# Optimization experiments

Hardware: AMD Instinct MI355X
Metric: run time of the kernel (lower is better)

The kernel has to match this reference:

```python
import jax, jax.numpy as jnp
import numpy as np
import math

D = 1024      # hidden_size
H = 16        # num_heads
HD = D // H   # head_dim = 64
ROPE = 64     # rope_dim == head_dim (full-head rotation, empty pass-through)
E = 8         # num_experts
F = 2560
BASE = 10000.0
EPS = 1e-5
SPECIALS = jnp.arange(2, 8)  # special_tokens indices {2..7} used as global tokens


def _ln(x, w, b):
    m = x.mean(-1, keepdims=True)
    v = x.var(-1, keepdims=True)  # biased var, matches torch LayerNorm
    return (x - m) / jnp.sqrt(v + EPS) * w + b


def _rope(x, cos, sin):
    # x: [B,H,T,HD]; rotate first ROPE dims via half-split (NOT rotate-half interleave)
    x1, x2 = x[..., : ROPE // 2], x[..., ROPE // 2 : ROPE]
    rot = jnp.concatenate([x1 * cos - x2 * sin, x1 * sin + x2 * cos], axis=-1)
    return jnp.concatenate([rot, x[..., ROPE:]], axis=-1)


def setup_inputs() -> dict:
    key = jax.random.key(0)
    ks = jax.random.split(key, 8)
    B, T = 1, 1024
    g = lambda k, shape, s: (jax.random.normal(k, shape, jnp.float32) * s)
    return {
        "x": g(ks[0], (B, T, D), 1.0),
        "input_ids": jax.random.randint(ks[1], (B, T), 0, 32000),
        "ln1_w": jnp.ones((D,), jnp.float32), "ln1_b": jnp.zeros((D,), jnp.float32),
        "qkv_w": g(ks[2], (D, 3 * D), 0.02), "qkv_b": jnp.zeros((3 * D,), jnp.float32),
        "attn_out_w": g(ks[3], (D, D), 0.02), "attn_out_b": jnp.zeros((D,), jnp.float32),
        "ln2_w": jnp.ones((D,), jnp.float32), "ln2_b": jnp.zeros((D,), jnp.float32),
        "gate_w": g(ks[4], (D, E), 0.02), "gate_b": jnp.zeros((E,), jnp.float32),
        "fc_w": g(ks[5], (E, D, 2 * F), 0.02), "fc_b": jnp.zeros((E, 2 * F), jnp.float32),
        "eout_w": g(ks[6], (E, F, D), 0.02), "eout_b": jnp.zeros((E, D), jnp.float32),
    }


def _block(x, input_ids, ln1_w, ln1_b, qkv_w, qkv_b, attn_out_w, attn_out_b,
           ln2_w, ln2_b, gate_w, gate_b, fc_w, fc_b, eout_w, eout_b):
    B, T, _ = x.shape
    # --- self-attention (pre-norm) ---
    h = _ln(x, ln1_w, ln1_b)
    qkv = h @ qkv_w + qkv_b
    q, k, v = jnp.split(qkv, 3, axis=-1)
    resh = lambda t: t.reshape(B, T, H, HD).transpose(0, 2, 1, 3)  # [B,H,T,HD]
    q, k, v = resh(q), resh(k), resh(v)
    pos = jnp.arange(T, dtype=jnp.float32)
    inv = 1.0 / (BASE ** (jnp.arange(0, ROPE, 2, dtype=jnp.float32) / ROPE))
    fr = pos[:, None] * inv[None, :]            # [T, ROPE/2]
    cos, sin = jnp.cos(fr), jnp.sin(fr)
    q = _rope(q, cos, sin)
    k = _rope(k, cos, sin)
    causal = jnp.tril(jnp.ones((T, T), bool))
    glob = (input_ids[..., None] == SPECIALS).any(-1)            # [B,T]
    allowed = causal[None, None] | glob[:, None, :, None]        # [B,1,T,T]
    logits = jnp.einsum('bhqd,bhkd->bhqk', q, k) / math.sqrt(HD)
    neg = -jnp.finfo(logits.dtype).max
    logits = jnp.where(allowed, logits, neg)
    aw = jax.nn.softmax(logits, axis=-1)
    attn = jnp.einsum('bhqk,bhkd->bhqd', aw, v).transpose(0, 2, 1, 3).reshape(B, T, H * HD)
    x = x + (attn @ attn_out_w + attn_out_b)
    # --- MoE GEGLU FFN (hard top-1 routing) ---
    h2 = _ln(x, ln2_w, ln2_b)
    gp = jax.nn.softmax(h2 @ gate_w + gate_b, axis=-1)           # [B,T,E]
    gw = gp.max(-1)
    gi = gp.argmax(-1)
    xf = h2.reshape(-1, D)
    gif = gi.reshape(-1)
    gwf = gw.reshape(-1)
    N = xf.shape[0]
    outf = jnp.zeros((N, D), x.dtype)
    for e in range(E):  # fixed small expert loop; select by routing mask
        h12 = xf @ fc_w[e] + fc_b[e]
        x1, x2 = h12[:, :F], h12[:, F:]
        y = (x1 * jax.nn.gelu(x2, approximate=False)) @ eout_w[e] + eout_b[e]
        outf = outf + jnp.where((gif == e)[:, None], y, 0.0)
    outf = outf * gwf[:, None]
    sums = jax.ops.segment_sum(gwf, gif, num_segments=E)
    counts = jax.ops.segment_sum(jnp.ones_like(gwf), gif, num_segments=E)
    usage = sums / (counts + 1e-8)
    moe_loss = jnp.sum((usage - 1.0 / E) ** 2)
    return x + outf.reshape(B, T, D), moe_loss


def reference(x, input_ids, ln1_w, ln1_b, qkv_w, qkv_b, attn_out_w, attn_out_b,
              ln2_w, ln2_b, gate_w, gate_b, fc_w, fc_b, eout_w, eout_b):
    return _block(x, input_ids, ln1_w, ln1_b, qkv_w, qkv_b, attn_out_w, attn_out_b,
                  ln2_w, ln2_b, gate_w, gate_b, fc_w, fc_b, eout_w, eout_b)
```

## Files before the change

### kernel.cpp

```cpp
#include <hip/hip_runtime.h>
#include <float.h>
#include <math.h>
#include <stdint.h>

#define T_ 1024
#define D_ 1024
#define H_ 16
#define HD_ 64
#define E_ 8
#define F_ 2560
#define D3_ 3072
#define F2_ 5120

#define WS_H    0u
#define WS_QKV  1048576u
#define WS_ATTN 4194304u
#define WS_X2   5242880u
#define WS_H2   6291456u
#define WS_A    7340032u
#define WS_GW   9961472u
#define WS_GI   9962496u
#define WS_OFFS 9963520u
#define WS_PERM 9963536u

typedef short short8 __attribute__((ext_vector_type(8)));
typedef short short4v __attribute__((ext_vector_type(4)));
typedef __bf16 bf16x8 __attribute__((ext_vector_type(8)));
typedef float floatx4 __attribute__((ext_vector_type(4)));

union FragU { short8 s; bf16x8 b; };

__device__ __forceinline__ short f2bf(float f) {
    union { float f; uint32_t u; } a; a.f = f;
    uint32_t r = a.u + 0x7fffu + ((a.u >> 16) & 1u);
    return (short)(r >> 16);
}

__device__ __forceinline__ void cvt16(const float4& a0, const float4& a1,
                                      const float4& a2, const float4& a3,
                                      short8& c0, short8& c1) {
    c0[0]=f2bf(a0.x); c0[1]=f2bf(a0.y); c0[2]=f2bf(a0.z); c0[3]=f2bf(a0.w);
    c0[4]=f2bf(a1.x); c0[5]=f2bf(a1.y); c0[6]=f2bf(a1.z); c0[7]=f2bf(a1.w);
    c1[0]=f2bf(a2.x); c1[1]=f2bf(a2.y); c1[2]=f2bf(a2.z); c1[3]=f2bf(a2.w);
    c1[4]=f2bf(a3.x); c1[5]=f2bf(a3.y); c1[6]=f2bf(a3.z); c1[7]=f2bf(a3.w);
}

#define GEMM_IDS \
    const int tid  = threadIdx.x;                 \
    const int a_m  = tid >> 1;                    \
    const int a_kh = (tid & 1) * 16;              \
    const int lane = tid & 63, wave = tid >> 6;   \
    const int wm = wave & 1,  wn = wave >> 1;     \
    const int quad = lane >> 4, lm = lane & 15;

__global__ __launch_bounds__(256) void gemm_mfma_full(
    const float* __restrict__ A, int lda,
    const float* __restrict__ B, int ldb,
    const float* __restrict__ bias,
    float* __restrict__ C, int ldc, int K)
{
    __shared__ __align__(16) short As[4*128*8];
    __shared__ __align__(16) short Bs[64*40];
    const int row0 = blockIdx.y * 128, col0 = blockIdx.x * 64;
    GEMM_IDS
    const int b_n = tid >> 2, b_kc = tid & 3;
    floatx4 acc[4][2];
    #pragma unroll
    for (int i=0;i<4;i++)
        #pragma unroll
        for (int j=0;j<2;j++) acc[i][j] = (floatx4){0.f,0.f,0.f,0.f};

    const float* apx = A + (size_t)(row0 + a_m) * lda + a_kh;
    const float* bpx = B + (size_t)(b_kc*8) * ldb + col0 + b_n;
    const int kcA = (tid & 1) * 2;

    float4 a0, a1, a2, a3; float bvv[8];
    a0 = *(const float4*)(apx);     a1 = *(const float4*)(apx + 4);
    a2 = *(const float4*)(apx + 8); a3 = *(const float4*)(apx + 12);
    #pragma unroll
    for (int j=0;j<8;j++) bvv[j] = bpx[(size_t)j*ldb];

    for (int k0 = 0; k0 < K; k0 += 32) {
        __syncthreads();
        short8 c0, c1, cb;
        cvt16(a0,a1,a2,a3,c0,c1);
        #pragma unroll
        for (int j=0;j<8;j++) cb[j] = f2bf(bvv[j]);
        *(short8*)&As[((kcA  )*128 + a_m)*8] = c0;
        *(short8*)&As[((kcA+1)*128 + a_m)*8] = c1;
        *(short8*)&Bs[b_n*40 + b_kc*8] = cb;
        __syncthreads();
        if (k0 + 32 < K) {
            const float* ap2 = apx + k0 + 32;
            a0 = *(const float4*)(ap2);     a1 = *(const float4*)(ap2 + 4);
            a2 = *(const float4*)(ap2 + 8); a3 = *(const float4*)(ap2 + 12);
            const float* bp2 = bpx + (size_t)(k0+32) * ldb;
            #pragma unroll
            for (int j=0;j<8;j++) bvv[j] = bp2[(size_t)j*ldb];
        }
        FragU fa[4], fb[2];
        #pragma unroll
        for (int i=0;i<4;i++) fa[i].s = *(short8*)&As[(quad*128 + wm*64 + i*16 + lm)*8];
        #pragma unroll
        for (int j=0;j<2;j++) fb[j].s = *(short8*)&Bs[(wn*32 + j*16 + lm)*40 + quad*8];
        #pragma unroll
        for (int i=0;i<4;i++)
            #pragma unroll
            for (int j=0;j<2;j++)
                acc[i][j] = __builtin_amdgcn_mfma_f32_16x16x32_bf16(fa[i].b, fb[j].b, acc[i][j], 0,0,0);
    }
    #pragma unroll
    for (int i=0;i<4;i++)
        #pragma unroll
        for (int j=0;j<2;j++) {
            int col = col0 + wn*32 + j*16 + lm;
            float bb = bias ? bias[col] : 0.f;
            #pragma unroll
            for (int r=0;r<4;r++) {
                int row = row0 + wm*64 + i*16 + quad*4 + r;
                C[(size_t)row*ldc + col] = acc[i][j][r] + bb;
            }
        }
}

__global__ __launch_bounds__(256) void gemm_mfma_acc(
    const float* __restrict__ A, int lda,
    const float* __restrict__ B, int ldb, long sB,
    const int* __restrict__ offs, const int* __restrict__ perm,
    float* __restrict__ Cacc, int ldc, int K, int nsk)
{
    const int sk = blockIdx.z % nsk;
    const int e  = blockIdx.z / nsk;
    int off = 0, Ne = T_;
    if (offs) { off = offs[e]; Ne = offs[e+1] - off; }
    const int row0 = blockIdx.y * 128;
    if (row0 >= Ne) return;
    const int col0 = blockIdx.x * 64;
    B += (long)e * sB;

    __shared__ __align__(16) short As[4*128*8];
    __shared__ __align__(16) short Bs[64*40];
    __shared__ int toks[128];
    GEMM_IDS
    const int b_n = tid >> 2, b_kc = tid & 3;
    if (tid < 128) {
        int r = row0 + tid;
        toks[tid] = offs ? ((r < Ne) ? perm[off + r] : -1) : r;
    }
    __syncthreads();

    floatx4 acc[4][2];
    #pragma unroll
    for (int i=0;i<4;i++)
        #pragma unroll
        for (int j=0;j<2;j++) acc[i][j] = (floatx4){0.f,0.f,0.f,0.f};

    const int tokA = toks[a_m];
    const float* apx = (tokA >= 0) ? (A + (size_t)tokA * lda + a_kh) : nullptr;
    const float* bpx = B + (size_t)(b_kc*8) * ldb + col0 + b_n;
    const int kcA = (tid & 1) * 2;
    const int Kp = K / nsk;
    const int koff = sk * Kp, kend = koff + Kp;

    float4 a0, a1, a2, a3; float bvv[8];
    a0 = make_float4(0,0,0,0); a1 = a0; a2 = a0; a3 = a0;
    if (apx) {
        a0 = *(const float4*)(apx + koff);     a1 = *(const float4*)(apx + koff + 4);
        a2 = *(const float4*)(apx + koff + 8); a3 = *(const float4*)(apx + koff + 12);
    }
    {
        const float* bp2 = bpx + (size_t)koff * ldb;
        #pragma unroll
        for (int j=0;j<8;j++) bvv[j] = bp2[(size_t)j*ldb];
    }

    for (int k0 = koff; k0 < kend; k0 += 32) {
        __syncthreads();
        short8 c0, c1, cb;
        cvt16(a0,a1,a2,a3,c0,c1);
        #pragma unroll
        for (int j=0;j<8;j++) cb[j] = f2bf(bvv[j]);
        *(short8*)&As[((kcA  )*128 + a_m)*8] = c0;
        *(short8*)&As[((kcA+1)*128 + a_m)*8] = c1;
        *(short8*)&Bs[b_n*40 + b_kc*8] = cb;
        __syncthreads();
        if (k0 + 32 < kend) {
            if (apx) {
                const float* ap2 = apx + k0 + 32;
                a0 = *(const float4*)(ap2);     a1 = *(const float4*)(ap2 + 4);
                a2 = *(const float4*)(ap2 + 8); a3 = *(const float4*)(ap2 + 12);
            }
            const float* bp2 = bpx + (size_t)(k0+32) * ldb;
            #pragma unroll
            for (int j=0;j<8;j++) bvv[j] = bp2[(size_t)j*ldb];
        }
        FragU fa[4], fb[2];
        #pragma unroll
        for (int i=0;i<4;i++) fa[i].s = *(short8*)&As[(quad*128 + wm*64 + i*16 + lm)*8];
        #pragma unroll
        for (int j=0;j<2;j++) fb[j].s = *(short8*)&Bs[(wn*32 + j*16 + lm)*40 + quad*8];
        #pragma unroll
        for (int i=0;i<4;i++)
            #pragma unroll
            for (int j=0;j<2;j++)
                acc[i][j] = __builtin_amdgcn_mfma_f32_16x16x32_bf16(fa[i].b, fb[j].b, acc[i][j], 0,0,0);
    }
    #pragma unroll
    for (int i=0;i<4;i++)
        #pragma unroll
        for (int j=0;j<2;j++) {
            int col = col0 + wn*32 + j*16 + lm;
            #pragma unroll
            for (int r=0;r<4;r++) {
                int tk = toks[wm*64 + i*16 + quad*4 + r];
                if (tk >= 0) atomicAdd(&Cacc[(size_t)tk*ldc + col], acc[i][j][r]);
            }
        }
}

__global__ __launch_bounds__(256) void moe_fc_mfma(
    const float* __restrict__ h2, const float* __restrict__ fcw,
    const float* __restrict__ fcb, const int* __restrict__ offs,
    const int* __restrict__ perm, float* __restrict__ aout)
{
    const int e = blockIdx.z;
    const int off = offs[e];
    const int Ne = offs[e+1] - off;
    const int row0 = blockIdx.y * 128;
    if (row0 >= Ne) return;
    const int col0 = blockIdx.x * 32;

    __shared__ __align__(16) short As[4*128*8];
    __shared__ __align__(16) short B1s[32*40];
    __shared__ __align__(16) short B2s[32*40];
    __shared__ int toks[128];
    GEMM_IDS
    const int n_l = tid & 31, kg = tid >> 5;
    if (tid < 128) {
        int r = row0 + tid;
        toks[tid] = (r < Ne) ? perm[off + r] : -1;
    }
    __syncthreads();

    floatx4 acc1[4], acc2[4];
    #pragma unroll
    for (int i=0;i<4;i++) {
        acc1[i] = (floatx4){0.f,0.f,0.f,0.f};
        acc2[i] = (floatx4){0.f,0.f,0.f,0.f};
    }

    const float* W = fcw + (size_t)e * D_ * F2_;
    const int tokA = toks[a_m];
    const float* apx = (tokA >= 0) ? (h2 + (size_t)tokA * D_ + a_kh) : nullptr;
    const float* bpx = W + (size_t)(kg*4) * F2_ + col0 + n_l;
    const int kcA = (tid & 1) * 2;

    float4 a0, a1, a2, a3; float b1v[4], b2v[4];
    a0 = make_float4(0,0,0,0); a1 = a0; a2 = a0; a3 = a0;
    if (apx) {
        a0 = *(const float4*)(apx);     a1 = *(const float4*)(apx + 4);
        a2 = *(const float4*)(apx + 8); a3 = *(const float4*)(apx + 12);
    }
    #pragma unroll
    for (int j=0;j<4;j++) { b1v[j] = bpx[(size_t)j*F2_]; b2v[j] = bpx[(size_t)j*F2_ + F_]; }

    for (int k0 = 0; k0 < D_; k0 += 32) {
        __syncthreads();
        short8 c0, c1;
        short4v cb1, cb2;
        cvt16(a0,a1,a2,a3,c0,c1);
        #pragma unroll
        for (int j=0;j<4;j++) { cb1[j] = f2bf(b1v[j]); cb2[j] = f2bf(b2v[j]); }
        *(short8*)&As[((kcA  )*128 + a_m)*8] = c0;
        *(short8*)&As[((kcA+1)*128 + a_m)*8] = c1;
        *(short4v*)&B1s[n_l*40 + kg*4] = cb1;
        *(short4v*)&B2s[n_l*40 + kg*4] = cb2;
        __syncthreads();
        if (k0 + 32 < D_) {
            if (apx) {
                const float* ap2 = apx + k0 + 32;
                a0 = *(const float4*)(ap2);     a1 = *(const float4*)(ap2 + 4);
                a2 = *(const float4*)(ap2 + 8); a3 = *(const float4*)(ap2 + 12);
            }
            const float* bp2 = bpx + (size_t)(k0+32) * F2_;
            #pragma unroll
            for (int j=0;j<4;j++) { b1v[j] = bp2[(size_t)j*F2_]; b2v[j] = bp2[(size_t)j*F2_ + F_]; }
        }
        FragU fa[4], fb1, fb2;
        #pragma unroll
        for (int i=0;i<4;i++) fa[i].s = *(short8*)&As[(quad*128 + wm*64 + i*16 + lm)*8];
        fb1.s = *(short8*)&B1s[(wn*16 + lm)*40 + quad*8];
        fb2.s = *(short8*)&B2s[(wn*16 + lm)*40 + quad*8];
        #pragma unroll
        for (int i=0;i<4;i++) {
            acc1[i] = __builtin_amdgcn_mfma_f32_16x16x32_bf16(fa[i].b, fb1.b, acc1[i], 0,0,0);
            acc2[i] = __builtin_amdgcn_mfma_f32_16x16x32_bf16(fa[i].b, fb2.b, acc2[i], 0,0,0);
        }
    }
    {
        int col = col0 + wn*16 + lm;
        float b1 = fcb[(size_t)e*F2_ + col];
        float b2 = fcb[(size_t)e*F2_ + F_ + col];
        #pragma unroll
        for (int i=0;i<4;i++)
            #pragma unroll
            for (int r=0;r<4;r++) {
                int tk = toks[wm*64 + i*16 + quad*4 + r];
                if (tk < 0) continue;
                float v1 = acc1[i][r] + b1;
                float v2 = acc2[i][r] + b2;
                float g = v2 * 0.5f * (1.0f + erff(v2 * 0.70710678118654752f));
                aout[(size_t)tk*F_ + col] = v1 * g;
            }
    }
}

__global__ __launch_bounds__(128) void flash_attn(
    const float* __restrict__ qkv, const int* __restrict__ ids,
    float* __restrict__ attnout)
{
    const int h  = blockIdx.y;
    const int q0 = blockIdx.x * 32;
    const int tid = threadIdx.x;
    const int lane = tid & 63, w = tid >> 6;
    const int quad = lane >> 4, lm = lane & 15;

    __shared__ __align__(16) short Qs[32*72];
    __shared__ __align__(16) short Ks[64*72];
    __shared__ __align__(16) short Vt[64*72];
    __shared__ __align__(16) short Ps[2][16*72];
    __shared__ int globf[32];

    {
        int row = tid >> 2, c = (tid & 3) * 16;
        const float* qp = qkv + (size_t)(q0 + row) * D3_ + h * HD_ + c;
        float4 f0 = *(const float4*)(qp);
        float4 f1 = *(const float4*)(qp + 4);
        float4 f2 = *(const float4*)(qp + 8);
        float4 f3 = *(const float4*)(qp + 12);
        short8 s0, s1;
        cvt16(f0, f1, f2, f3, s0, s1);
        *(short8*)&Qs[row*72 + c]     = s0;
        *(short8*)&Qs[row*72 + c + 8] = s1;
    }
    if (tid < 32) {
        int id = ids[q0 + tid];
        globf[tid] = (id >= 2 && id <= 7) ? 1 : 0;
    }
    __syncthreads();

    FragU QA[2];
    #pragma unroll
    for (int s = 0; s < 2; s++)
        QA[s].s = *(short8*)&Qs[(w*16 + lm)*72 + s*32 + quad*8];

    int any = 0;
    #pragma unroll
    for (int i = 0; i < 32; i++) any |= globf[i];
    const int nt = any ? (T_/64) : ((q0 + 31) >> 6) + 1;

    int gq[4]; int qidx[4];
    #pragma unroll
    for (int r = 0; r < 4; r++) {
        int ql = w*16 + quad*4 + r;
        qidx[r] = q0 + ql;
        gq[r] = globf[ql];
    }

    float mrow[4] = {-1e30f, -1e30f, -1e30f, -1e30f};
    float lrow[4] = {0.f, 0.f, 0.f, 0.f};
    floatx4 Oacc[4];
    #pragma unroll
    for (int n = 0; n < 4; n++) Oacc[n] = (floatx4){0.f, 0.f, 0.f, 0.f};

    for (int kt = 0; kt < nt; kt++) {
        __syncthreads();
        #pragma unroll
        for (int rep = 0; rep < 2; rep++) {
            int key = (tid >> 2) + rep*32;
            int c = (tid & 3) * 16;
            const float* kp = qkv + (size_t)(kt*64 + key) * D3_ + D_ + h*HD_ + c;
            float4 f0 = *(const float4*)(kp);
            float4 f1 = *(const float4*)(kp + 4);
            float4 f2 = *(const float4*)(kp + 8);
            float4 f3 = *(const float4*)(kp + 12);
            short8 s0, s1;
            cvt16(f0, f1, f2, f3, s0, s1);
            *(short8*)&Ks[key*72 + c]     = s0;
            *(short8*)&Ks[key*72 + c + 8] = s1;
        }
        #pragma unroll
        for (int rep = 0; rep < 8; rep++) {
            int lin = tid + rep*128;
            int key = lin >> 4;
            int c = (lin & 15) * 4;
            const float* vp = qkv + (size_t)(kt*64 + key) * D3_ + 2*D_ + h*HD_ + c;
            float4 f = *(const float4*)vp;
            Vt[(c+0)*72 + key] = f2bf(f.x);
            Vt[(c+1)*72 + key] = f2bf(f.y);
            Vt[(c+2)*72 + key] = f2bf(f.z);
            Vt[(c+3)*72 + key] = f2bf(f.w);
        }
        __syncthreads();

        floatx4 Sv[4];
        #pragma unroll
        for (int n = 0; n < 4; n++) {
            Sv[n] = (floatx4){0.f, 0.f, 0.f, 0.f};
            #pragma unroll
            for (int s = 0; s < 2; s++) {
                FragU KB;
                KB.s = *(short8*)&Ks[(n*16 + lm)*72 + s*32 + quad*8];
                Sv[n] = __builtin_amdgcn_mfma_f32_16x16x32_bf16(QA[s].b, KB.b, Sv[n], 0, 0, 0);
            }
        }
        #pragma unroll
        for (int n = 0; n < 4; n++) {
            int key = kt*64 + n*16 + lm;
            #pragma unroll
            for (int r = 0; r < 4; r++) {
                float v = Sv[n][r] * 0.125f;
                if (!gq[r] && key > qidx[r]) v = -1e30f;
                Sv[n][r] = v;
            }
        }
        float mnew[4], alpha[4], tsum[4];
        #pragma unroll
        for (int r = 0; r < 4; r++) {
            float tm = fmaxf(fmaxf(Sv[0][r], Sv[1][r]), fmaxf(Sv[2][r], Sv[3][r]));
            #pragma unroll
            for (int x = 1; x < 16; x <<= 1) tm = fmaxf(tm, __shfl_xor(tm, x));
            mnew[r] = fmaxf(mrow[r], tm);
            alpha[r] = __expf(mrow[r] - mnew[r]);
            mrow[r] = mnew[r];
            tsum[r] = 0.f;
        }
        #pragma unroll
        for (int n = 0; n < 4; n++) {
            #pragma unroll
            for (int r = 0; r < 4; r++) {
                float p = __expf(Sv[n][r] - mnew[r]);
                tsum[r] += p;
                Ps[w][(quad*4 + r)*72 + n*16 + lm] = f2bf(p);
            }
        }
        #pragma unroll
        for (int r = 0; r < 4; r++) {
            #pragma unroll
            for (int x = 1; x < 16; x <<= 1) tsum[r] += __shfl_xor(tsum[r], x);
            lrow[r] = lrow[r] * alpha[r] + tsum[r];
        }
        #pragma unroll
        for (int n = 0; n < 4; n++)
            #pragma unroll
            for (int r = 0; r < 4; r++) Oacc[n][r] *= alpha[r];

        #pragma unroll
        for (int s = 0; s < 2; s++) {
            FragU PA;
            PA.s = *(short8*)&Ps[w][lm*72 + s*32 + quad*8];
            #pragma unroll
            for (int n = 0; n < 4; n++) {
                FragU VB;
                VB.s = *(short8*)&Vt[(n*16 + lm)*72 + s*32 + quad*8];
                Oacc[n] = __builtin_amdgcn_mfma_f32_16x16x32_bf16(PA.b, VB.b, Oacc[n], 0, 0, 0);
            }
        }
    }

    #pragma unroll
    for (int n = 0; n < 4; n++)
        #pragma unroll
        for (int r = 0; r < 4; r++) {
            float o = Oacc[n][r] / lrow[r];
            attnout[(size_t)qidx[r]*D_ + h*HD_ + n*16 + lm] = o;
        }
}

__global__ __launch_bounds__(256) void ep_attn(
    const float* __restrict__ x, const float* __restrict__ sacc,
    const float* __restrict__ aob, float* __restrict__ x2)
{
    int row = blockIdx.x, tid = threadIdx.x;
    float4 xv = ((const float4*)(x + (size_t)row*D_))[tid];
    float4 sv = ((const float4*)(sacc + (size_t)row*D_))[tid];
    float4 bv = ((const float4*)aob)[tid];
    float4 o;
    o.x = xv.x + sv.x + bv.x; o.y = xv.y + sv.y + bv.y;
    o.z = xv.z + sv.z + bv.z; o.w = xv.w + sv.w + bv.w;
    ((float4*)(x2 + (size_t)row*D_))[tid] = o;
}

__global__ __launch_bounds__(256) void ep_moe(
    const float* __restrict__ x2, const float* __restrict__ sacc,
    const float* __restrict__ eob, const float* __restrict__ gw,
    const int* __restrict__ gi, float* __restrict__ out)
{
    int row = blockIdx.x, tid = threadIdx.x;
    float g = gw[row];
    int e = gi[row];
    float4 xv = ((const float4*)(x2 + (size_t)row*D_))[tid];
    float4 sv = ((const float4*)(sacc + (size_t)row*D_))[tid];
    float4 bv = ((const float4*)(eob + (size_t)e*D_))[tid];
    float4 o;
    o.x = xv.x + g*(sv.x + bv.x); o.y = xv.y + g*(sv.y + bv.y);
    o.z = xv.z + g*(sv.z + bv.z); o.w = xv.w + g*(sv.w + bv.w);
    ((float4*)(out + (size_t)row*D_))[tid] = o;
}

__global__ __launch_bounds__(256) void ln_kernel(
    const float* __restrict__ x, const float* __restrict__ w,
    const float* __restrict__ b, float* __restrict__ out)
{
    const int row = blockIdx.x, tid = threadIdx.x;
    const int lane = tid & 63, wave = tid >> 6;
    float4 v = ((const float4*)(x + (size_t)row * D_))[tid];
    float s  = v.x + v.y + v.z + v.w;
    float sq = v.x*v.x + v.y*v.y + v.z*v.z + v.w*v.w;
    #pragma unroll
    for (int off = 32; off; off >>= 1) {
        s  += __shfl_down(s, off);
        sq += __shfl_down(sq, off);
    }
    __shared__ float rs[4], rq[4], mv[2];
    if (lane == 0) { rs[wave] = s; rq[wave] = sq; }
    __syncthreads();
    if (tid == 0) {
        float ts = rs[0]+rs[1]+rs[2]+rs[3];
        float tq = rq[0]+rq[1]+rq[2]+rq[3];
        float mean = ts * (1.0f / D_);
        float var  = tq * (1.0f / D_) - mean*mean;
        mv[0] = mean; mv[1] = rsqrtf(var + 1e-5f);
    }
    __syncthreads();
    float mean = mv[0], rstd = mv[1];
    float4 wv = ((const float4*)w)[tid];
    float4 bv = ((const float4*)b)[tid];
    float4 o;
    o.x = (v.x-mean)*rstd*wv.x + bv.x;
    o.y = (v.y-mean)*rstd*wv.y + bv.y;
    o.z = (v.z-mean)*rstd*wv.z + bv.z;
    o.w = (v.w-mean)*rstd*wv.w + bv.w;
    ((float4*)(out + (size_t)row * D_))[tid] = o;
}

__global__ __launch_bounds__(256) void rope_kernel(float* __restrict__ qkv)
{
    int gid = blockIdx.x * 256 + threadIdx.x;
    int t = gid >> 9;
    int r = gid & 511;
    int h = r >> 5;
    int d = r & 31;
    float inv = powf(10000.0f, -(float)d * (1.0f/32.0f));
    float fr = (float)t * inv;
    float s, c;
    sincosf(fr, &s, &c);
    float* base = qkv + (size_t)t*D3_ + h*HD_ + d;
    float q1 = base[0], q2 = base[32];
    base[0]  = q1*c - q2*s;
    base[32] = q1*s + q2*c;
    float* kb = base + D_;
    float k1 = kb[0], k2 = kb[32];
    kb[0]  = k1*c - k2*s;
    kb[32] = k1*s + k2*c;
}

__global__ __launch_bounds__(256) void ln2_gate_kernel(
    const float* __restrict__ x2, const float* __restrict__ w,
    const float* __restrict__ b, const float* __restrict__ gwm,
    const float* __restrict__ gbv, float* __restrict__ h2,
    int* __restrict__ gi, float* __restrict__ gw)
{
    const int row = blockIdx.x, tid = threadIdx.x;
    const int lane = tid & 63, wave = tid >> 6;
    float4 v = ((const float4*)(x2 + (size_t)row * D_))[tid];
    float s  = v.x + v.y + v.z + v.w;
    float sq = v.x*v.x + v.y*v.y + v.z*v.z + v.w*v.w;
    #pragma unroll
    for (int off = 32; off; off >>= 1) {
        s  += __shfl_down(s, off);
        sq += __shfl_down(sq, off);
    }
    __shared__ float rs[4], rq[4], mv[2];
    if (lane == 0) { rs[wave] = s; rq[wave] = sq; }
    __syncthreads();
    if (tid == 0) {
        float ts = rs[0]+rs[1]+rs[2]+rs[3];
        float tq = rq[0]+rq[1]+rq[2]+rq[3];
        float mean = ts * (1.0f / D_);
        float var  = tq * (1.0f / D_) - mean*mean;
        mv[0] = mean; mv[1] = rsqrtf(var + 1e-5f);
    }
    __syncthreads();
    float mean = mv[0], rstd = mv[1];
    float4 wv = ((const float4*)w)[tid];
    float4 bv = ((const float4*)b)[tid];
    float hv[4];
    hv[0] = (v.x-mean)*rstd*wv.x + bv.x;
    hv[1] = (v.y-mean)*rstd*wv.y + bv.y;
    hv[2] = (v.z-mean)*rstd*wv.z + bv.z;
    hv[3] = (v.w-mean)*rstd*wv.w + bv.w;
    float4 o; o.x=hv[0]; o.y=hv[1]; o.z=hv[2]; o.w=hv[3];
    ((float4*)(h2 + (size_t)row * D_))[tid] = o;

    float acc[E_] = {};
    int c = tid * 4;
    #pragma unroll
    for (int j = 0; j < 4; j++) {
        const float* gr = gwm + (size_t)(c+j) * E_;
        #pragma unroll
        for (int e = 0; e < E_; e++) acc[e] += hv[j] * gr[e];
    }
    #pragma unroll
    for (int off = 32; off; off >>= 1)
        #pragma unroll
        for (int e = 0; e < E_; e++) acc[e] += __shfl_down(acc[e], off);
    __shared__ float gred[4][E_];
    if (lane == 0)
        for (int e = 0; e < E_; e++) gred[wave][e] = acc[e];
    __syncthreads();
    if (tid == 0) {
        float lg[E_];
        float mxl = -FLT_MAX; int mi = 0;
        for (int e = 0; e < E_; e++)
            lg[e] = gred[0][e]+gred[1][e]+gred[2][e]+gred[3][e] + gbv[e];
        for (int e = 0; e < E_; e++)
            if (lg[e] > mxl) { mxl = lg[e]; mi = e; }
        float ssum = 0.f;
        for (int e = 0; e < E_; e++) ssum += expf(lg[e] - mxl);
        gi[row] = mi;
        gw[row] = 1.0f / ssum;
    }
}

__global__ void route_kernel(const int* __restrict__ gi,
                             int* __restrict__ offs, int* __restrict__ perm)
{
    __shared__ int cnt[E_], c2[E_], off[E_+1];
    const int tid = threadIdx.x;
    if (tid < E_) { cnt[tid] = 0; c2[tid] = 0; }
    __syncthreads();
    int e = gi[tid];
    atomicAdd(&cnt[e], 1);
    __syncthreads();
    if (tid == 0) {
        off[0] = 0;
        for (int i = 0; i < E_; i++) off[i+1] = off[i] + cnt[i];
        for (int i = 0; i <= E_; i++) offs[i] = off[i];
    }
    __syncthreads();
    int r = atomicAdd(&c2[e], 1);
    perm[off[e] + r] = tid;
}

__global__ void loss_kernel(const int* __restrict__ gi,
                            const float* __restrict__ gw, float* __restrict__ out)
{
    __shared__ float ss[E_], sc[E_];
    const int tid = threadIdx.x;
    if (tid < E_) { ss[tid] = 0.f; sc[tid] = 0.f; }
    __syncthreads();
    for (int t = tid; t < T_; t += 256) {
        int e = gi[t];
        atomicAdd(&ss[e], gw[t]);
        atomicAdd(&sc[e], 1.0f);
    }
    __syncthreads();
    if (tid == 0) {
        float loss = 0.f;
        for (int e = 0; e < E_; e++) {
            float u = ss[e] / (sc[e] + 1e-8f);
            float d = u - 0.125f;
            loss += d * d;
        }
        out[(size_t)T_ * D_] = loss;
    }
}

extern "C" void kernel_launch(void* const* d_in, const int* in_sizes, int n_in,
                              void* d_out, int out_size, void* d_ws, size_t ws_size,
                              hipStream_t stream)
{
    const float* x     = (const float*)d_in[0];
    const int*   ids   = (const int*)d_in[1];
    const float* ln1w  = (const float*)d_in[2];
    const float* ln1b  = (const float*)d_in[3];
    const float* qkvw  = (const float*)d_in[4];
    const float* qkvb  = (const float*)d_in[5];
    const float* aow   = (const float*)d_in[6];
    const float* aob   = (const float*)d_in[7];
    const float* ln2w  = (const float*)d_in[8];
    const float* ln2b  = (const float*)d_in[9];
    const float* gatew = (const float*)d_in[10];
    const float* gateb = (const float*)d_in[11];
    const float* fcw   = (const float*)d_in[12];
    const float* fcb   = (const float*)d_in[13];
    const float* eoutw = (const float*)d_in[14];
    const float* eoutb = (const float*)d_in[15];
    float* out = (float*)d_out;
    float* ws  = (float*)d_ws;

    float* h    = ws + WS_H;
    float* sacc = ws + WS_H;
    float* qkv  = ws + WS_QKV;
    float* attn = ws + WS_ATTN;
    float* x2   = ws + WS_X2;
    float* h2   = ws + WS_H2;
    float* abuf = ws + WS_A;
    float* gw   = ws + WS_GW;
    int*   gi   = (int*)(ws + WS_GI);
    int*   offs = (int*)(ws + WS_OFFS);
    int*   perm = (int*)(ws + WS_PERM);

    ln_kernel<<<T_, 256, 0, stream>>>(x, ln1w, ln1b, h);
    gemm_mfma_full<<<dim3(D3_/64, T_/128), 256, 0, stream>>>(
        h, D_, qkvw, D3_, qkvb, qkv, D3_, D_);
    rope_kernel<<<(T_*H_*32)/256, 256, 0, stream>>>(qkv);
    flash_attn<<<dim3(T_/32, H_), 128, 0, stream>>>(qkv, ids, attn);
    hipMemsetAsync(sacc, 0, (size_t)T_*D_*sizeof(float), stream);
    gemm_mfma_acc<<<dim3(D_/64, T_/128, 4), 256, 0, stream>>>(
        attn, D_, aow, D_, 0, nullptr, nullptr, sacc, D_, D_, 4);
    ep_attn<<<T_, 256, 0, stream>>>(x, sacc, aob, x2);
    ln2_gate_kernel<<<T_, 256, 0, stream>>>(x2, ln2w, ln2b, gatew, gateb, h2, gi, gw);
    route_kernel<<<1, T_, 0, stream>>>(gi, offs, perm);
    moe_fc_mfma<<<dim3(F_/32, T_/128, E_), 256, 0, stream>>>(h2, fcw, fcb, offs, perm, abuf);
    hipMemsetAsync(sacc, 0, (size_t)T_*D_*sizeof(float), stream);
    gemm_mfma_acc<<<dim3(D_/64, T_/128, 4*E_), 256, 0, stream>>>(
        abuf, F_, eoutw, D_, (long)F_*D_, offs, perm, sacc, D_, F_, 4);
    ep_moe<<<T_, 256, 0, stream>>>(x2, sacc, eoutb, gw, gi, out);
    loss_kernel<<<1, 256, 0, stream>>>(gi, gw, out);
}
```

Before: 592.6 us.

## Use wide 128x256 MFMA tiles for QKV and MoE GEMMs, split-K partials

Replaces the QKV projection and both MoE expert GEMMs with new kernels that use 128x256 output tiles per block, row-major padded LDS staging and an XOR swizzle on the B tile. Each block now does more MFMA work per loaded A and B element. The MoE output projection no longer uses atomicAdd into a zeroed buffer: it writes four split-K partial buffers that ep_moe2 sums, which drops a memset and the atomic traffic. In exchange, register pressure per block rises and the partials reuse the dead QKV workspace region.

```diff
diff --git a/kernel.cpp b/kernel.cpp
--- a/kernel.cpp
+++ b/kernel.cpp
@@ -22,9 +22,9 @@
 #define WS_GI   9962496u
 #define WS_OFFS 9963520u
 #define WS_PERM 9963536u
+#define WS_PART 0u
 
 typedef short short8 __attribute__((ext_vector_type(8)));
-typedef short short4v __attribute__((ext_vector_type(4)));
 typedef __bf16 bf16x8 __attribute__((ext_vector_type(8)));
 typedef float floatx4 __attribute__((ext_vector_type(4)));
 
@@ -45,6 +45,254 @@
     c1[4]=f2bf(a3.x); c1[5]=f2bf(a3.y); c1[6]=f2bf(a3.z); c1[7]=f2bf(a3.w);
 }
 
+
+#define W_IDS \
+    const int tid = threadIdx.x;                   \
+    const int lane = tid & 63, wv = tid >> 6;      \
+    const int wm = wv & 1, wn = wv >> 1;           \
+    const int quad = lane >> 4, lm = lane & 15;    \
+    const int am = tid >> 1, akh = (tid & 1) * 16;
+
+#define A_STORE(AP, AR) {                                          \
+    short8 s0, s1;                                                 \
+    if (AP) cvt16(AR[0], AR[1], AR[2], AR[3], s0, s1);             \
+    else { s0 = (short8){0,0,0,0,0,0,0,0}; s1 = s0; }              \
+    *(short8*)&As[am*40 + akh]     = s0;                           \
+    *(short8*)&As[am*40 + akh + 8] = s1; }
+
+#define B_STORE(BR) {                                              \
+    uint32_t* Bu = (uint32_t*)Bs;                                  \
+    _Pragma("unroll")                                              \
+    for (int s = 0; s < 4; s++) {                                  \
+        int r0 = s*8 + wv*2;                                       \
+        _Pragma("unroll")                                          \
+        for (int i = 0; i < 4; i++) {                              \
+            uint32_t pk = (uint32_t)(unsigned short)f2bf(((const float*)&BR[2*s])[i]) \
+                 | ((uint32_t)(unsigned short)f2bf(((const float*)&BR[2*s+1])[i]) << 16); \
+            Bu[(4*lane + i)*20 + ((r0 >> 1) ^ ((lane & 3) << 2))] = pk; \
+        } } }
+
+#define B_LOAD(BR, BP, ROWOFF, LDB) {                              \
+    _Pragma("unroll")                                              \
+    for (int s = 0; s < 4; s++) {                                  \
+        int r0 = s*8 + wv*2;                                       \
+        BR[2*s]   = *(const float4*)(BP + (size_t)(ROWOFF + r0) * LDB);     \
+        BR[2*s+1] = *(const float4*)(BP + (size_t)(ROWOFF + r0 + 1) * LDB); \
+    } }
+
+#define A_LOAD(AR, AP, KOFF) {                                     \
+    if (AP) { _Pragma("unroll")                                    \
+        for (int i = 0; i < 4; i++) AR[i] = *(const float4*)(AP + (KOFF) + i*4); } }
+
+__global__ __launch_bounds__(256, 2) void qkv_w(
+    const float* __restrict__ h, const float* __restrict__ qkvw,
+    const float* __restrict__ qkvb, float* __restrict__ qkv)
+{
+    const int col0 = blockIdx.x * 256;
+    const int y0 = blockIdx.y * 128;
+    __shared__ __align__(16) short As[128*40];
+    __shared__ __align__(16) short Bs[256*40];
+    W_IDS
+
+    floatx4 acc[4][8];
+    #pragma unroll
+    for (int i=0;i<4;i++)
+        #pragma unroll
+        for (int j=0;j<8;j++) acc[i][j] = (floatx4){0.f,0.f,0.f,0.f};
+
+    const float* ap = h + (size_t)(y0 + am)*D_ + akh;
+    const float* bp = qkvw + col0 + 4*lane;
+
+    float4 aR[4], bR[8];
+    A_LOAD(aR, ap, 0)
+    B_LOAD(bR, bp, 0, D3_)
+
+    for (int k0 = 0; k0 < D_; k0 += 32) {
+        __syncthreads();
+        A_STORE(ap, aR)
+        B_STORE(bR)
+        __syncthreads();
+        if (k0 + 32 < D_) {
+            A_LOAD(aR, ap, k0 + 32)
+            B_LOAD(bR, bp, k0 + 32, D3_)
+        }
+        FragU fa[4], fb[8];
+        #pragma unroll
+        for (int i=0;i<4;i++) fa[i].s = *(short8*)&As[(wm*64 + i*16 + lm)*40 + quad*8];
+        const int kk = (quad*8) ^ (((lm>>2)&3)<<3);
+        #pragma unroll
+        for (int j=0;j<8;j++) fb[j].s = *(short8*)&Bs[(wn*128 + j*16 + lm)*40 + kk];
+        #pragma unroll
+        for (int i=0;i<4;i++)
+            #pragma unroll
+            for (int j=0;j<8;j++)
+                acc[i][j] = __builtin_amdgcn_mfma_f32_16x16x32_bf16(fa[i].b, fb[j].b, acc[i][j], 0,0,0);
+    }
+    #pragma unroll
+    for (int j=0;j<8;j++) {
+        int col = col0 + wn*128 + j*16 + lm;
+        float bb = qkvb[col];
+        #pragma unroll
+        for (int i=0;i<4;i++)
+            #pragma unroll
+            for (int r=0;r<4;r++) {
+                int tok = y0 + wm*64 + i*16 + quad*4 + r;
+                qkv[(size_t)tok*D3_ + col] = acc[i][j][r] + bb;
+            }
+    }
+}
+
+__global__ __launch_bounds__(256, 2) void moe_fc_w(
+    const float* __restrict__ h2, const float* __restrict__ fcw,
+    const float* __restrict__ fcb, const int* __restrict__ offs,
+    const int* __restrict__ perm, float* __restrict__ aout)
+{
+    const int e = blockIdx.z;
+    const int off = offs[e], Ne = offs[e+1] - off;
+    const int y0 = blockIdx.y * 128;
+    if (y0 >= Ne) return;
+    const int col0 = blockIdx.x * 128;
+
+    __shared__ __align__(16) short As[128*40];
+    __shared__ __align__(16) short Bs[256*40];
+    __shared__ int toks[128];
+    W_IDS
+    if (tid < 128) {
+        int r = y0 + tid;
+        toks[tid] = (r < Ne) ? perm[off + r] : -1;
+    }
+    __syncthreads();
+
+    floatx4 acc[4][8];
+    #pragma unroll
+    for (int i=0;i<4;i++)
+        #pragma unroll
+        for (int j=0;j<8;j++) acc[i][j] = (floatx4){0.f,0.f,0.f,0.f};
+
+    const int tokA = toks[am];
+    const float* ap = (tokA >= 0) ? (h2 + (size_t)tokA*D_ + akh) : nullptr;
+    const int gcol = (lane < 32) ? (col0 + 4*lane) : (F_ + col0 + 4*lane - 128);
+    const float* bp = fcw + (size_t)e*D_*F2_ + gcol;
+
+    float4 aR[4] = {}, bR[8];
+    A_LOAD(aR, ap, 0)
+    B_LOAD(bR, bp, 0, F2_)
+
+    for (int k0 = 0; k0 < D_; k0 += 32) {
+        __syncthreads();
+        A_STORE(ap, aR)
+        B_STORE(bR)
+        __syncthreads();
+        if (k0 + 32 < D_) {
+            A_LOAD(aR, ap, k0 + 32)
+            B_LOAD(bR, bp, k0 + 32, F2_)
+        }
+        FragU fa[4], fb[8];
+        #pragma unroll
+        for (int i=0;i<4;i++) fa[i].s = *(short8*)&As[(wm*64 + i*16 + lm)*40 + quad*8];
+        const int kk = (quad*8) ^ (((lm>>2)&3)<<3);
+        #pragma unroll
+        for (int j=0;j<4;j++) {
+            fb[j].s   = *(short8*)&Bs[(wn*64 + j*16 + lm)*40 + kk];
+            fb[j+4].s = *(short8*)&Bs[(128 + wn*64 + j*16 + lm)*40 + kk];
+        }
+        #pragma unroll
+        for (int i=0;i<4;i++)
+            #pragma unroll
+            for (int j=0;j<8;j++)
+                acc[i][j] = __builtin_amdgcn_mfma_f32_16x16x32_bf16(fa[i].b, fb[j].b, acc[i][j], 0,0,0);
+    }
+    #pragma unroll
+    for (int j=0;j<4;j++) {
+        int col = col0 + wn*64 + j*16 + lm;
+        float b1 = fcb[(size_t)e*F2_ + col];
+        float b2 = fcb[(size_t)e*F2_ + F_ + col];
+        #pragma unroll
+        for (int i=0;i<4;i++)
+            #pragma unroll
+            for (int r=0;r<4;r++) {
+                int tk = toks[wm*64 + i*16 + quad*4 + r];
+                if (tk < 0) continue;
+                float v1 = acc[i][j][r] + b1;
+                float v2 = acc[i][j+4][r] + b2;
+                float g = v2 * 0.5f * (1.0f + erff(v2 * 0.70710678118654752f));
+                aout[(size_t)tk*F_ + col] = v1 * g;
+            }
+    }
+}
+
+__global__ __launch_bounds__(256, 2) void moe_out_w(
+    const float* __restrict__ abuf, const float* __restrict__ ew,
+    const int* __restrict__ offs, const int* __restrict__ perm,
+    float* __restrict__ part)
+{
+    const int e  = blockIdx.z >> 2;
+    const int sk = blockIdx.z & 3;
+    const int off = offs[e], Ne = offs[e+1] - off;
+    const int y0 = blockIdx.y * 128;
+    if (y0 >= Ne) return;
+    const int col0 = blockIdx.x * 256;
+
+    __shared__ __align__(16) short As[128*40];
+    __shared__ __align__(16) short Bs[256*40];
+    __shared__ int toks[128];
+    W_IDS
+    if (tid < 128) {
+        int r = y0 + tid;
+        toks[tid] = (r < Ne) ? perm[off + r] : -1;
+    }
+    __syncthreads();
+
+    floatx4 acc[4][8];
+    #pragma unroll
+    for (int i=0;i<4;i++)
+        #pragma unroll
+        for (int j=0;j<8;j++) acc[i][j] = (floatx4){0.f,0.f,0.f,0.f};
+
+    const int tokA = toks[am];
+    const float* ap = (tokA >= 0) ? (abuf + (size_t)tokA*F_ + akh) : nullptr;
+    const float* bp = ew + (size_t)e*F_*D_ + col0 + 4*lane;
+    const int koff = sk * (F_/4), kend = koff + (F_/4);
+
+    float4 aR[4] = {}, bR[8];
+    A_LOAD(aR, ap, koff)
+    B_LOAD(bR, bp, koff, D_)
+
+    for (int k0 = koff; k0 < kend; k0 += 32) {
+        __syncthreads();
+        A_STORE(ap, aR)
+        B_STORE(bR)
+        __syncthreads();
+        if (k0 + 32 < kend) {
+            A_LOAD(aR, ap, k0 + 32)
+            B_LOAD(bR, bp, k0 + 32, D_)
+        }
+        FragU fa[4], fb[8];
+        #pragma unroll
+        for (int i=0;i<4;i++) fa[i].s = *(short8*)&As[(wm*64 + i*16 + lm)*40 + quad*8];
+        const int kk = (quad*8) ^ (((lm>>2)&3)<<3);
+        #pragma unroll
+        for (int j=0;j<8;j++) fb[j].s = *(short8*)&Bs[(wn*128 + j*16 + lm)*40 + kk];
+        #pragma unroll
+        for (int i=0;i<4;i++)
+            #pragma unroll
+            for (int j=0;j<8;j++)
+                acc[i][j] = __builtin_amdgcn_mfma_f32_16x16x32_bf16(fa[i].b, fb[j].b, acc[i][j], 0,0,0);
+    }
+    float* pb = part + (size_t)sk*T_*D_;
+    #pragma unroll
+    for (int j=0;j<8;j++) {
+        int col = col0 + wn*128 + j*16 + lm;
+        #pragma unroll
+        for (int i=0;i<4;i++)
+            #pragma unroll
+            for (int r=0;r<4;r++) {
+                int tk = toks[wm*64 + i*16 + quad*4 + r];
+                if (tk >= 0) pb[(size_t)tk*D_ + col] = acc[i][j][r];
+            }
+    }
+}
+
 #define GEMM_IDS \
     const int tid  = threadIdx.x;                 \
     const int a_m  = tid >> 1;                    \
@@ -53,17 +301,20 @@
     const int wm = wave & 1,  wn = wave >> 1;     \
     const int quad = lane >> 4, lm = lane & 15;
 
-__global__ __launch_bounds__(256) void gemm_mfma_full(
+__global__ __launch_bounds__(256) void gemm_mfma_acc(
     const float* __restrict__ A, int lda,
     const float* __restrict__ B, int ldb,
-    const float* __restrict__ bias,
-    float* __restrict__ C, int ldc, int K)
-{
+    float* __restrict__ Cacc, int ldc, int K, int nsk)
+{
+    const int sk = blockIdx.z;
+    const int row0 = blockIdx.y * 128;
+    const int col0 = blockIdx.x * 64;
+
     __shared__ __align__(16) short As[4*128*8];
     __shared__ __align__(16) short Bs[64*40];
-    const int row0 = blockIdx.y * 128, col0 = blockIdx.x * 64;
     GEMM_IDS
     const int b_n = tid >> 2, b_kc = tid & 3;
+
     floatx4 acc[4][2];
     #pragma unroll
     for (int i=0;i<4;i++)
@@ -73,14 +324,19 @@
     const float* apx = A + (size_t)(row0 + a_m) * lda + a_kh;
     const float* bpx = B + (size_t)(b_kc*8) * ldb + col0 + b_n;
     const int kcA = (tid & 1) * 2;
+    const int Kp = K / nsk;
+    const int koff = sk * Kp, kend = koff + Kp;
 
     float4 a0, a1, a2, a3; float bvv[8];
-    a0 = *(const float4*)(apx);     a1 = *(const float4*)(apx + 4);
-    a2 = *(const float4*)(apx + 8); a3 = *(const float4*)(apx + 12);
-    #pragma unroll
-    for (int j=0;j<8;j++) bvv[j] = bpx[(size_t)j*ldb];
-
-    for (int k0 = 0; k0 < K; k0 += 32) {
+    a0 = *(const float4*)(apx + koff);     a1 = *(const float4*)(apx + koff + 4);
+    a2 = *(const float4*)(apx + koff + 8); a3 = *(const float4*)(apx + koff + 12);
+    {
+        const float* bp2 = bpx + (size_t)koff * ldb;
+        #pragma unroll
+        for (int j=0;j<8;j++) bvv[j] = bp2[(size_t)j*ldb];
+    }
+
+    for (int k0 = koff; k0 < kend; k0 += 32) {
         __syncthreads();
         short8 c0, c1, cb;
         cvt16(a0,a1,a2,a3,c0,c1);
@@ -90,7 +346,7 @@
         *(short8*)&As[((kcA+1)*128 + a_m)*8] = c1;
         *(short8*)&Bs[b_n*40 + b_kc*8] = cb;
         __syncthreads();
-        if (k0 + 32 < K) {
+        if (k0 + 32 < kend) {
             const float* ap2 = apx + k0 + 32;
             a0 = *(const float4*)(ap2);     a1 = *(const float4*)(ap2 + 4);
             a2 = *(const float4*)(ap2 + 8); a3 = *(const float4*)(ap2 + 12);
@@ -114,205 +370,12 @@
         #pragma unroll
         for (int j=0;j<2;j++) {
             int col = col0 + wn*32 + j*16 + lm;
-            float bb = bias ? bias[col] : 0.f;
             #pragma unroll
             for (int r=0;r<4;r++) {
                 int row = row0 + wm*64 + i*16 + quad*4 + r;
-                C[(size_t)row*ldc + col] = acc[i][j][r] + bb;
+                atomicAdd(&Cacc[(size_t)row*ldc + col], acc[i][j][r]);
             }
         }
-}
-
-__global__ __launch_bounds__(256) void gemm_mfma_acc(
-    const float* __restrict__ A, int lda,
-    const float* __restrict__ B, int ldb, long sB,
-    const int* __restrict__ offs, const int* __restrict__ perm,
-    float* __restrict__ Cacc, int ldc, int K, int nsk)
-{
-    const int sk = blockIdx.z % nsk;
-    const int e  = blockIdx.z / nsk;
-    int off = 0, Ne = T_;
-    if (offs) { off = offs[e]; Ne = offs[e+1] - off; }
-    const int row0 = blockIdx.y * 128;
-    if (row0 >= Ne) return;
-    const int col0 = blockIdx.x * 64;
-    B += (long)e * sB;
-
-    __shared__ __align__(16) short As[4*128*8];
-    __shared__ __align__(16) short Bs[64*40];
-    __shared__ int toks[128];
-    GEMM_IDS
-    const int b_n = tid >> 2, b_kc = tid & 3;
-    if (tid < 128) {
-        int r = row0 + tid;
-        toks[tid] = offs ? ((r < Ne) ? perm[off + r] : -1) : r;
-    }
-    __syncthreads();
-
-    floatx4 acc[4][2];
-    #pragma unroll
-    for (int i=0;i<4;i++)
-        #pragma unroll
-        for (int j=0;j<2;j++) acc[i][j] = (floatx4){0.f,0.f,0.f,0.f};
-
-    const int tokA = toks[a_m];
-    const float* apx = (tokA >= 0) ? (A + (size_t)tokA * lda + a_kh) : nullptr;
-    const float* bpx = B + (size_t)(b_kc*8) * ldb + col0 + b_n;
-    const int kcA = (tid & 1) * 2;
-    const int Kp = K / nsk;
-    const int koff = sk * Kp, kend = koff + Kp;
-
-    float4 a0, a1, a2, a3; float bvv[8];
-    a0 = make_float4(0,0,0,0); a1 = a0; a2 = a0; a3 = a0;
-    if (apx) {
-        a0 = *(const float4*)(apx + koff);     a1 = *(const float4*)(apx + koff + 4);
-        a2 = *(const float4*)(apx + koff + 8); a3 = *(const float4*)(apx + koff + 12);
-    }
-    {
-        const float* bp2 = bpx + (size_t)koff * ldb;
-        #pragma unroll
-        for (int j=0;j<8;j++) bvv[j] = bp2[(size_t)j*ldb];
-    }
-
-    for (int k0 = koff; k0 < kend; k0 += 32) {
-        __syncthreads();
-        short8 c0, c1, cb;
-        cvt16(a0,a1,a2,a3,c0,c1);
-        #pragma unroll
-        for (int j=0;j<8;j++) cb[j] = f2bf(bvv[j]);
-        *(short8*)&As[((kcA  )*128 + a_m)*8] = c0;
-        *(short8*)&As[((kcA+1)*128 + a_m)*8] = c1;
-        *(short8*)&Bs[b_n*40 + b_kc*8] = cb;
-        __syncthreads();
-        if (k0 + 32 < kend) {
-            if (apx) {
-                const float* ap2 = apx + k0 + 32;
-                a0 = *(const float4*)(ap2);     a1 = *(const float4*)(ap2 + 4);
-                a2 = *(const float4*)(ap2 + 8); a3 = *(const float4*)(ap2 + 12);
-            }
-            const float* bp2 = bpx + (size_t)(k0+32) * ldb;
-            #pragma unroll
-            for (int j=0;j<8;j++) bvv[j] = bp2[(size_t)j*ldb];
-        }
-        FragU fa[4], fb[2];
-        #pragma unroll
-        for (int i=0;i<4;i++) fa[i].s = *(short8*)&As[(quad*128 + wm*64 + i*16 + lm)*8];
-        #pragma unroll
-        for (int j=0;j<2;j++) fb[j].s = *(short8*)&Bs[(wn*32 + j*16 + lm)*40 + quad*8];
-        #pragma unroll
-        for (int i=0;i<4;i++)
-            #pragma unroll
-            for (int j=0;j<2;j++)
-                acc[i][j] = __builtin_amdgcn_mfma_f32_16x16x32_bf16(fa[i].b, fb[j].b, acc[i][j], 0,0,0);
-    }
-    #pragma unroll
-    for (int i=0;i<4;i++)
-        #pragma unroll
-        for (int j=0;j<2;j++) {
-            int col = col0 + wn*32 + j*16 + lm;
-            #pragma unroll
-            for (int r=0;r<4;r++) {
-                int tk = toks[wm*64 + i*16 + quad*4 + r];
-                if (tk >= 0) atomicAdd(&Cacc[(size_t)tk*ldc + col], acc[i][j][r]);
-            }
-        }
-}
-
-__global__ __launch_bounds__(256) void moe_fc_mfma(
-    const float* __restrict__ h2, const float* __restrict__ fcw,
-    const float* __restrict__ fcb, const int* __restrict__ offs,
-    const int* __restrict__ perm, float* __restrict__ aout)
-{
-    const int e = blockIdx.z;
-    const int off = offs[e];
-    const int Ne = offs[e+1] - off;
-    const int row0 = blockIdx.y * 128;
-    if (row0 >= Ne) return;
-    const int col0 = blockIdx.x * 32;
-
-    __shared__ __align__(16) short As[4*128*8];
-    __shared__ __align__(16) short B1s[32*40];
-    __shared__ __align__(16) short B2s[32*40];
-    __shared__ int toks[128];
-    GEMM_IDS
-    const int n_l = tid & 31, kg = tid >> 5;
-    if (tid < 128) {
-        int r = row0 + tid;
-        toks[tid] = (r < Ne) ? perm[off + r] : -1;
-    }
-    __syncthreads();
-
-    floatx4 acc1[4], acc2[4];
-    #pragma unroll
-    for (int i=0;i<4;i++) {
-        acc1[i] = (floatx4){0.f,0.f,0.f,0.f};
-        acc2[i] = (floatx4){0.f,0.f,0.f,0.f};
-    }
-
-    const float* W = fcw + (size_t)e * D_ * F2_;
-    const int tokA = toks[a_m];
-    const float* apx = (tokA >= 0) ? (h2 + (size_t)tokA * D_ + a_kh) : nullptr;
-    const float* bpx = W + (size_t)(kg*4) * F2_ + col0 + n_l;
-    const int kcA = (tid & 1) * 2;
-
-    float4 a0, a1, a2, a3; float b1v[4], b2v[4];
-    a0 = make_float4(0,0,0,0); a1 = a0; a2 = a0; a3 = a0;
-    if (apx) {
-        a0 = *(const float4*)(apx);     a1 = *(const float4*)(apx + 4);
-        a2 = *(const float4*)(apx + 8); a3 = *(const float4*)(apx + 12);
-    }
-    #pragma unroll
-    for (int j=0;j<4;j++) { b1v[j] = bpx[(size_t)j*F2_]; b2v[j] = bpx[(size_t)j*F2_ + F_]; }
-
-    for (int k0 = 0; k0 < D_; k0 += 32) {
-        __syncthreads();
-        short8 c0, c1;
-        short4v cb1, cb2;
-        cvt16(a0,a1,a2,a3,c0,c1);
-        #pragma unroll
-        for (int j=0;j<4;j++) { cb1[j] = f2bf(b1v[j]); cb2[j] = f2bf(b2v[j]); }
-        *(short8*)&As[((kcA  )*128 + a_m)*8] = c0;
-        *(short8*)&As[((kcA+1)*128 + a_m)*8] = c1;
-        *(short4v*)&B1s[n_l*40 + kg*4] = cb1;
-        *(short4v*)&B2s[n_l*40 + kg*4] = cb2;
-        __syncthreads();
-        if (k0 + 32 < D_) {
-            if (apx) {
-                const float* ap2 = apx + k0 + 32;
-                a0 = *(const float4*)(ap2);     a1 = *(const float4*)(ap2 + 4);
-                a2 = *(const float4*)(ap2 + 8); a3 = *(const float4*)(ap2 + 12);
-            }
-            const float* bp2 = bpx + (size_t)(k0+32) * F2_;
-            #pragma unroll
-            for (int j=0;j<4;j++) { b1v[j] = bp2[(size_t)j*F2_]; b2v[j] = bp2[(size_t)j*F2_ + F_]; }
-        }
-        FragU fa[4], fb1, fb2;
-        #pragma unroll
-        for (int i=0;i<4;i++) fa[i].s = *(short8*)&As[(quad*128 + wm*64 + i*16 + lm)*8];
-        fb1.s = *(short8*)&B1s[(wn*16 + lm)*40 + quad*8];
-        fb2.s = *(short8*)&B2s[(wn*16 + lm)*40 + quad*8];
-        #pragma unroll
-        for (int i=0;i<4;i++) {
-            acc1[i] = __builtin_amdgcn_mfma_f32_16x16x32_bf16(fa[i].b, fb1.b, acc1[i], 0,0,0);
-            acc2[i] = __builtin_amdgcn_mfma_f32_16x16x32_bf16(fa[i].b, fb2.b, acc2[i], 0,0,0);
-        }
-    }
-    {
-        int col = col0 + wn*16 + lm;
-        float b1 = fcb[(size_t)e*F2_ + col];
-        float b2 = fcb[(size_t)e*F2_ + F_ + col];
-        #pragma unroll
-        for (int i=0;i<4;i++)
-            #pragma unroll
-            for (int r=0;r<4;r++) {
-                int tk = toks[wm*64 + i*16 + quad*4 + r];
-                if (tk < 0) continue;
-                float v1 = acc1[i][r] + b1;
-                float v2 = acc2[i][r] + b2;
-                float g = v2 * 0.5f * (1.0f + erff(v2 * 0.70710678118654752f));
-                aout[(size_t)tk*F_ + col] = v1 * g;
-            }
-    }
 }
 
 __global__ __launch_bounds__(128) void flash_attn(
@@ -491,8 +554,8 @@
     ((float4*)(x2 + (size_t)row*D_))[tid] = o;
 }
 
-__global__ __launch_bounds__(256) void ep_moe(
-    const float* __restrict__ x2, const float* __restrict__ sacc,
+__global__ __launch_bounds__(256) void ep_moe2(
+    const float* __restrict__ x2, const float* __restrict__ part,
     const float* __restrict__ eob, const float* __restrict__ gw,
     const int* __restrict__ gi, float* __restrict__ out)
 {
@@ -500,11 +563,16 @@
     float g = gw[row];
     int e = gi[row];
     float4 xv = ((const float4*)(x2 + (size_t)row*D_))[tid];
-    float4 sv = ((const float4*)(sacc + (size_t)row*D_))[tid];
+    float4 s0 = ((const float4*)(part + 0ul*T_*D_ + (size_t)row*D_))[tid];
+    float4 s1 = ((const float4*)(part + 1ul*T_*D_ + (size_t)row*D_))[tid];
+    float4 s2 = ((const float4*)(part + 2ul*T_*D_ + (size_t)row*D_))[tid];
+    float4 s3 = ((const float4*)(part + 3ul*T_*D_ + (size_t)row*D_))[tid];
     float4 bv = ((const float4*)(eob + (size_t)e*D_))[tid];
     float4 o;
-    o.x = xv.x + g*(sv.x + bv.x); o.y = xv.y + g*(sv.y + bv.y);
-    o.z = xv.z + g*(sv.z + bv.z); o.w = xv.w + g*(sv.w + bv.w);
+    o.x = xv.x + g*(s0.x+s1.x+s2.x+s3.x + bv.x);
+    o.y = xv.y + g*(s0.y+s1.y+s2.y+s3.y + bv.y);
+    o.z = xv.z + g*(s0.z+s1.z+s2.z+s3.z + bv.z);
+    o.w = xv.w + g*(s0.w+s1.w+s2.w+s3.w + bv.w);
     ((float4*)(out + (size_t)row*D_))[tid] = o;
 }
 
@@ -702,6 +770,7 @@
 
     float* h    = ws + WS_H;
     float* sacc = ws + WS_H;
+    float* part = ws + WS_PART;
     float* qkv  = ws + WS_QKV;
     float* attn = ws + WS_ATTN;
     float* x2   = ws + WS_X2;
@@ -713,20 +782,17 @@
     int*   perm = (int*)(ws + WS_PERM);
 
     ln_kernel<<<T_, 256, 0, stream>>>(x, ln1w, ln1b, h);
-    gemm_mfma_full<<<dim3(D3_/64, T_/128), 256, 0, stream>>>(
-        h, D_, qkvw, D3_, qkvb, qkv, D3_, D_);
+    qkv_w<<<dim3(D3_/256, T_/128), 256, 0, stream>>>(h, qkvw, qkvb, qkv);
     rope_kernel<<<(T_*H_*32)/256, 256, 0, stream>>>(qkv);
     flash_attn<<<dim3(T_/32, H_), 128, 0, stream>>>(qkv, ids, attn);
     hipMemsetAsync(sacc, 0, (size_t)T_*D_*sizeof(float), stream);
     gemm_mfma_acc<<<dim3(D_/64, T_/128, 4), 256, 0, stream>>>(
-        attn, D_, aow, D_, 0, nullptr, nullptr, sacc, D_, D_, 4);
+        attn, D_, aow, D_, sacc, D_, D_, 4);
     ep_attn<<<T_, 256, 0, stream>>>(x, sacc, aob, x2);
     ln2_gate_kernel<<<T_, 256, 0, stream>>>(x2, ln2w, ln2b, gatew, gateb, h2, gi, gw);
     route_kernel<<<1, T_, 0, stream>>>(gi, offs, perm);
-    moe_fc_mfma<<<dim3(F_/32, T_/128, E_), 256, 0, stream>>>(h2, fcw, fcb, offs, perm, abuf);
-    hipMemsetAsync(sacc, 0, (size_t)T_*D_*sizeof(float), stream);
-    gemm_mfma_acc<<<dim3(D_/64, T_/128, 4*E_), 256, 0, stream>>>(
-        abuf, F_, eoutw, D_, (long)F_*D_, offs, perm, sacc, D_, F_, 4);
-    ep_moe<<<T_, 256, 0, stream>>>(x2, sacc, eoutb, gw, gi, out);
+    moe_fc_w<<<dim3(F_/128, T_/128, E_), 256, 0, stream>>>(h2, fcw, fcb, offs, perm, abuf);
+    moe_out_w<<<dim3(D_/256, T_/128, 4*E_), 256, 0, stream>>>(abuf, eoutw, offs, perm, part);
+    ep_moe2<<<T_, 256, 0, stream>>>(x2, part, eoutb, gw, gi, out);
     loss_kernel<<<1, 256, 0, stream>>>(gi, gw, out);
 }
```

Result: slower. 643.0 us (+8.5%).
